# Performance work log

Hardware: AMD Instinct MI355X
Metric: run time of the kernel (lower is better)

The kernel has to match this reference:

```python
import jax, jax.numpy as jnp
import numpy as np

NUM_GLOBAL_EXPERTS = 256
LOCAL_START = 64  # global experts [64, 128) live on this rank


def setup_inputs() -> dict:
    key = jax.random.key(0)
    k1, = jax.random.split(key, 1)
    num_local_experts = 64
    # Routing ids: ~4.2M tokens x topk=8, values are GLOBAL expert ids in [0, 256)
    topk_ids = jax.random.randint(k1, (33554432,), 0, NUM_GLOBAL_EXPERTS, dtype=jnp.int32)
    # expert_map: global -> local; -1 for experts not owned by this rank
    gid = jnp.arange(NUM_GLOBAL_EXPERTS, dtype=jnp.int32)
    expert_map = jnp.where(
        (gid >= LOCAL_START) & (gid < LOCAL_START + num_local_experts),
        gid - LOCAL_START,
        jnp.int32(-1),
    )
    return {"topk_ids": topk_ids, "num_local_experts": num_local_experts, "expert_map": expert_map}


def reference(topk_ids, num_local_experts, expert_map=None):
    n = num_local_experts  # static python int
    ids = topk_ids.reshape(-1)
    if expert_map is not None:
        # invalid ids (< 0) stay invalid; valid global ids are remapped to local space
        ids = jnp.where(ids >= 0, expert_map[jnp.clip(ids, 0)], jnp.int32(-1))
    # Route all invalid / out-of-range ids into an overflow bucket n, then drop it.
    valid = (ids >= 0) & (ids < n)
    bucket = jnp.where(valid, ids, jnp.int32(n))
    counts = jax.ops.segment_sum(
        jnp.ones_like(bucket, dtype=jnp.int32), bucket, num_segments=n + 1
    )
    return counts[:n].astype(jnp.int32)
```

## Files before the change

kernel.cpp:

```cpp
#include <hip/hip_runtime.h>

#define BLOCK   256
#define NB1     2048
#define NBINS   256
#define NWAVES  (BLOCK / 64)
#define UNROLL  4

__global__ __launch_bounds__(BLOCK) void hist_part(const int* __restrict__ ids,
                                                   int N,
                                                   const int* __restrict__ emap,
                                                   int emap_n,
                                                   int* __restrict__ partials,
                                                   int n_local) {
    __shared__ int hist[NWAVES * NBINS];
    __shared__ int lmap[NBINS];
    __shared__ int s_lo, s_cnt, s_ok;
    const int tid = threadIdx.x;

    if (tid == 0) { s_lo = 0x7FFFFFFF; s_cnt = 0; s_ok = 1; }
    for (int i = tid; i < NWAVES * NBINS; i += BLOCK) hist[i] = 0;
    __syncthreads();

    for (int g = tid; g < NBINS; g += BLOCK) {
        int m = (g < emap_n) ? emap[g] : -1;
        lmap[g] = m;
        if (m >= 0) { atomicMin(&s_lo, g); atomicAdd(&s_cnt, 1); }
    }
    __syncthreads();
    const int lo = s_lo;
    const unsigned cnt = (unsigned)s_cnt;
    for (int g = tid; g < NBINS; g += BLOCK) {
        int expect = (g >= lo && (unsigned)(g - lo) < cnt) ? (g - lo) : -1;
        if (lmap[g] != expect) s_ok = 0;
    }
    __syncthreads();
    const int affine = s_ok;

    int* h = &hist[(tid >> 6) * NBINS];

    const int4* __restrict__ ids4 = (const int4*)ids;
    const int n4      = N >> 2;
    const int chunk   = BLOCK * UNROLL;
    const int gstride = (int)gridDim.x * chunk;
    const int n4_full = (n4 / gstride) * gstride;

    if (affine) {
        for (int i = (int)blockIdx.x * chunk + tid; i < n4_full; i += gstride) {
            int4 v[UNROLL];
#pragma unroll
            for (int u = 0; u < UNROLL; ++u) v[u] = ids4[i + u * BLOCK];
#pragma unroll
            for (int u = 0; u < UNROLL; ++u) {
                unsigned a = (unsigned)(v[u].x - lo);
                unsigned b = (unsigned)(v[u].y - lo);
                unsigned c = (unsigned)(v[u].z - lo);
                unsigned d = (unsigned)(v[u].w - lo);
                if (a < cnt) atomicAdd(&h[a], 1);
                if (b < cnt) atomicAdd(&h[b], 1);
                if (c < cnt) atomicAdd(&h[c], 1);
                if (d < cnt) atomicAdd(&h[d], 1);
            }
        }
        for (int i = n4_full + (int)blockIdx.x * BLOCK + tid; i < n4;
             i += (int)gridDim.x * BLOCK) {
            int4 v = ids4[i];
            unsigned a = (unsigned)(v.x - lo), b = (unsigned)(v.y - lo);
            unsigned c = (unsigned)(v.z - lo), d = (unsigned)(v.w - lo);
            if (a < cnt) atomicAdd(&h[a], 1);
            if (b < cnt) atomicAdd(&h[b], 1);
            if (c < cnt) atomicAdd(&h[c], 1);
            if (d < cnt) atomicAdd(&h[d], 1);
        }
        if (blockIdx.x == 0) {
            for (int i = (n4 << 2) + tid; i < N; i += BLOCK) {
                unsigned a = (unsigned)(ids[i] - lo);
                if (a < cnt) atomicAdd(&h[a], 1);
            }
        }
    } else {
        for (int i = (int)blockIdx.x * chunk + tid; i < n4_full; i += gstride) {
            int4 v[UNROLL];
#pragma unroll
            for (int u = 0; u < UNROLL; ++u) v[u] = ids4[i + u * BLOCK];
#pragma unroll
            for (int u = 0; u < UNROLL; ++u) {
                int l0 = ((unsigned)v[u].x < NBINS) ? lmap[v[u].x] : -1;
                int l1 = ((unsigned)v[u].y < NBINS) ? lmap[v[u].y] : -1;
                int l2 = ((unsigned)v[u].z < NBINS) ? lmap[v[u].z] : -1;
                int l3 = ((unsigned)v[u].w < NBINS) ? lmap[v[u].w] : -1;
                if (l0 >= 0) atomicAdd(&h[l0], 1);
                if (l1 >= 0) atomicAdd(&h[l1], 1);
                if (l2 >= 0) atomicAdd(&h[l2], 1);
                if (l3 >= 0) atomicAdd(&h[l3], 1);
            }
        }
        for (int i = n4_full + (int)blockIdx.x * BLOCK + tid; i < n4;
             i += (int)gridDim.x * BLOCK) {
            int4 v = ids4[i];
            int l0 = ((unsigned)v.x < NBINS) ? lmap[v.x] : -1;
            int l1 = ((unsigned)v.y < NBINS) ? lmap[v.y] : -1;
            int l2 = ((unsigned)v.z < NBINS) ? lmap[v.z] : -1;
            int l3 = ((unsigned)v.w < NBINS) ? lmap[v.w] : -1;
            if (l0 >= 0) atomicAdd(&h[l0], 1);
            if (l1 >= 0) atomicAdd(&h[l1], 1);
            if (l2 >= 0) atomicAdd(&h[l2], 1);
            if (l3 >= 0) atomicAdd(&h[l3], 1);
        }
        if (blockIdx.x == 0) {
            for (int i = (n4 << 2) + tid; i < N; i += BLOCK) {
                int v = ids[i];
                int l = ((unsigned)v < NBINS) ? lmap[v] : -1;
                if (l >= 0) atomicAdd(&h[l], 1);
            }
        }
    }
    __syncthreads();

    for (int b = tid; b < n_local; b += BLOCK) {
        int s = 0;
#pragma unroll
        for (int w = 0; w < NWAVES; ++w) s += hist[w * NBINS + b];
        partials[b * NB1 + blockIdx.x] = s;
    }
}

__global__ __launch_bounds__(BLOCK) void reduce_part(const int* __restrict__ partials,
                                                     int* __restrict__ out) {
    const int b = blockIdx.x;
    const int tid = threadIdx.x;
    int s = 0;
    for (int j = tid; j < NB1; j += BLOCK) s += partials[b * NB1 + j];
#pragma unroll
    for (int off = 32; off > 0; off >>= 1) s += __shfl_down(s, off, 64);
    __shared__ int wsum[NWAVES];
    if ((tid & 63) == 0) wsum[tid >> 6] = s;
    __syncthreads();
    if (tid == 0) {
        int tot = 0;
#pragma unroll
        for (int w = 0; w < NWAVES; ++w) tot += wsum[w];
        out[b] = tot;
    }
}

extern "C" void kernel_launch(void* const* d_in, const int* in_sizes, int n_in,
                              void* d_out, int out_size, void* d_ws, size_t ws_size,
                              hipStream_t stream) {
    const int* topk_ids   = (const int*)d_in[0];
    const int* expert_map = (const int*)d_in[2];
    const int N       = in_sizes[0];
    const int emap_n  = in_sizes[2];
    const int n_local = out_size;

    int* partials = (int*)d_ws;

    hist_part<<<NB1, BLOCK, 0, stream>>>(topk_ids, N, expert_map, emap_n,
                                         partials, n_local);
    reduce_part<<<n_local, BLOCK, 0, stream>>>(partials, (int*)d_out);
}
```

Before: 194.0 us.

## Fuse histogram reduction into one kernel using global 64-bit paired atomics

Replaces the two-kernel partials-plus-reduce scheme with a single histogram kernel. Each block folds its per-wave histograms in shared memory and adds them to the zeroed output with 64-bit atomics that update two adjacent counters at once. Block size grows to 512 and the grid shrinks to 512 blocks. This removes the second launch and the partials write and read-back, but adds a memset, global atomic contention, and a 64-bit paired add whose low counter could carry into the high one. The paired add also assumes the output buffer is 8-byte aligned.

After: 197.0 us. No clear change (+1.5%).

```diff
diff --git a/kernel.cpp b/kernel.cpp
--- a/kernel.cpp
+++ b/kernel.cpp
@@ -1,19 +1,20 @@
 #include <hip/hip_runtime.h>
 
-#define BLOCK   256
-#define NB1     2048
+#define BLOCK   512
+#define NBLK    512
 #define NBINS   256
 #define NWAVES  (BLOCK / 64)
 #define UNROLL  4
 
-__global__ __launch_bounds__(BLOCK) void hist_part(const int* __restrict__ ids,
-                                                   int N,
-                                                   const int* __restrict__ emap,
-                                                   int emap_n,
-                                                   int* __restrict__ partials,
-                                                   int n_local) {
+__global__ __launch_bounds__(BLOCK) void hist_fused(const int* __restrict__ ids,
+                                                    int N,
+                                                    const int* __restrict__ emap,
+                                                    int emap_n,
+                                                    int* __restrict__ out,
+                                                    int n_local) {
     __shared__ int hist[NWAVES * NBINS];
     __shared__ int lmap[NBINS];
+    __shared__ int fold[NBINS];
     __shared__ int s_lo, s_cnt, s_ok;
     const int tid = threadIdx.x;
 
@@ -120,26 +121,20 @@
         int s = 0;
 #pragma unroll
         for (int w = 0; w < NWAVES; ++w) s += hist[w * NBINS + b];
-        partials[b * NB1 + blockIdx.x] = s;
+        fold[b] = s;
     }
-}
+    __syncthreads();
 
-__global__ __launch_bounds__(BLOCK) void reduce_part(const int* __restrict__ partials,
-                                                     int* __restrict__ out) {
-    const int b = blockIdx.x;
-    const int tid = threadIdx.x;
-    int s = 0;
-    for (int j = tid; j < NB1; j += BLOCK) s += partials[b * NB1 + j];
-#pragma unroll
-    for (int off = 32; off > 0; off >>= 1) s += __shfl_down(s, off, 64);
-    __shared__ int wsum[NWAVES];
-    if ((tid & 63) == 0) wsum[tid >> 6] = s;
-    __syncthreads();
-    if (tid == 0) {
-        int tot = 0;
-#pragma unroll
-        for (int w = 0; w < NWAVES; ++w) tot += wsum[w];
-        out[b] = tot;
+    const int npair = n_local >> 1;
+    for (int p = tid; p < npair; p += BLOCK) {
+        unsigned long long v =
+            (unsigned long long)(unsigned)fold[2 * p] |
+            ((unsigned long long)(unsigned)fold[2 * p + 1] << 32);
+        if (v) atomicAdd((unsigned long long*)out + p, v);
+    }
+    if ((n_local & 1) && tid == 0) {
+        int s = fold[n_local - 1];
+        if (s) atomicAdd(&out[n_local - 1], s);
     }
 }
 
@@ -152,9 +147,7 @@
     const int emap_n  = in_sizes[2];
     const int n_local = out_size;
 
-    int* partials = (int*)d_ws;
-
-    hist_part<<<NB1, BLOCK, 0, stream>>>(topk_ids, N, expert_map, emap_n,
-                                         partials, n_local);
-    reduce_part<<<n_local, BLOCK, 0, stream>>>(partials, (int*)d_out);
+    hipMemsetAsync(d_out, 0, (size_t)n_local * sizeof(int), stream);
+    hist_fused<<<NBLK, BLOCK, 0, stream>>>(topk_ids, N, expert_map, emap_n,
+                                           (int*)d_out, n_local);
 }
```
